# Performance work log

Hardware: AMD Instinct MI355X
Metric: run time of the kernel (lower is better)

The kernel has to match this reference:

```python
import jax, jax.numpy as jnp
import numpy as np

N = 50000    # nodes
E = 600000   # edges
F = 128      # num_features
ED = 16      # edge_dim
H = 4        # heads
D = 32       # per-head channels = hidden_units // heads
HID = H * D  # hidden_units = 128
C = 10       # num_classes


def _lin(k, fan_in, fan_out):
    # torch.nn.Linear-style init scale
    return jax.random.uniform(k, (fan_in, fan_out), jnp.float32, -1.0, 1.0) / np.sqrt(fan_in)


def setup_inputs() -> dict:
    key = jax.random.key(0)
    ks = jax.random.split(key, 24)
    inp = {
        "x": jax.random.normal(ks[0], (N, F), jnp.float32),
        "edge_index": jax.random.randint(ks[1], (2, E), 0, N, dtype=jnp.int32),
        "edge_attr": jax.random.normal(ks[2], (E, ED), jnp.float32),
    }
    j = 3
    for l, ind in enumerate([F, HID]):
        specs = {"q": (ind, HID, True), "k": (ind, HID, True), "v": (ind, HID, True),
                 "e": (ED, HID, False), "s": (ind, HID, True)}
        for nm, (i, o, bias) in specs.items():
            inp[f"W{nm}{l}"] = _lin(ks[j], i, o); j += 1
            if bias:
                inp[f"b{nm}{l}"] = jnp.zeros((o,), jnp.float32)
    inp["Wout"] = _lin(ks[j], HID, C)
    inp["bout"] = jnp.zeros((C,), jnp.float32)
    return inp


def _transformer_conv(x, src, dst, eattr, Wq, bq, Wk, bk, Wv, bv, We, Ws, bs):
    # PyG TransformerConv: concat=True, root_weight=True, beta=False, eval dropout.
    n = x.shape[0]
    q = (x @ Wq + bq).reshape(n, H, D)
    k = (x @ Wk + bk).reshape(n, H, D)
    v = (x @ Wv + bv).reshape(n, H, D)
    e = (eattr @ We).reshape(-1, H, D)           # edge embedding, added to key and value
    kj = k[src] + e                              # [E, H, D]
    vj = v[src] + e                              # [E, H, D]
    logits = jnp.einsum("ehd,ehd->eh", q[dst], kj) / np.sqrt(D)
    m = jax.ops.segment_max(logits, dst, num_segments=n)          # [N, H]
    ex = jnp.exp(logits - m[dst])
    denom = jax.ops.segment_sum(ex, dst, num_segments=n)          # [N, H]
    alpha = ex / (denom[dst] + 1e-16)                             # PyG softmax eps
    out = jax.ops.segment_sum(vj * alpha[..., None], dst, num_segments=n)
    return out.reshape(n, HID) + x @ Ws + bs                      # concat heads + skip


def reference(x, edge_index, edge_attr,
              Wq0, bq0, Wk0, bk0, Wv0, bv0, We0, Ws0, bs0,
              Wq1, bq1, Wk1, bk1, Wv1, bv1, We1, Ws1, bs1,
              Wout, bout):
    src, dst = edge_index[0], edge_index[1]
    h = jax.nn.relu(_transformer_conv(x, src, dst, edge_attr,
                                      Wq0, bq0, Wk0, bk0, Wv0, bv0, We0, Ws0, bs0))
    h = jax.nn.relu(_transformer_conv(h, src, dst, edge_attr,
                                      Wq1, bq1, Wk1, bk1, Wv1, bv1, We1, Ws1, bs1))
    logits = h @ Wout + bout
    return jax.nn.log_softmax(logits, axis=1)
```

## Files before the change

### kernel.cpp

```cpp
#include <hip/hip_runtime.h>

typedef unsigned short u16;
typedef unsigned int u32;
typedef __attribute__((ext_vector_type(4))) u16 u16x4;
typedef __attribute__((ext_vector_type(8))) u16 u16x8;
typedef __attribute__((ext_vector_type(4))) u32 u32x4;
typedef __attribute__((ext_vector_type(8))) short short8;
typedef __attribute__((ext_vector_type(4))) float f32x4;
typedef __attribute__((ext_vector_type(4))) float f4;
typedef __attribute__((ext_vector_type(2))) float f2;

#define NN 50000
#define NE 600000
#define HEADS 4
#define DH 32
#define HIDU 128
#define NC 10
#define NBLK 196
#define WES_T 34
#define WES_H 546

#define SCALE2 0.25503486164f

__device__ __forceinline__ float bf2f(u16 u) {
    union { unsigned int i; float f; } c; c.i = ((unsigned int)u) << 16; return c.f;
}
__device__ __forceinline__ u16 f2bf(float f) {
    union { float f; unsigned int i; } c; c.f = f;
    unsigned int x = c.i;
    return (u16)((x + 0x7fffu + ((x >> 16) & 1u)) >> 16);
}
__device__ __forceinline__ float lo_bf(u32 d) { return __uint_as_float(d << 16); }
__device__ __forceinline__ float hi_bf(u32 d) { return __uint_as_float(d & 0xffff0000u); }
__device__ __forceinline__ float qadd_xor1(float v) {
    int o = __builtin_amdgcn_update_dpp(0, __float_as_int(v), 0xB1, 0xF, 0xF, true);
    return v + __int_as_float(o);
}
__device__ __forceinline__ float qadd_xor2(float v) {
    int o = __builtin_amdgcn_update_dpp(0, __float_as_int(v), 0x4E, 0xF, 0xF, true);
    return v + __int_as_float(o);
}

__global__ void k_zero(int* p, int n) {
    int i = blockIdx.x * blockDim.x + threadIdx.x;
    if (i < n) p[i] = 0;
}

__global__ void k_hist(const int* __restrict__ dst, int* __restrict__ deg) {
    int i = blockIdx.x * blockDim.x + threadIdx.x;
    if (i < NE) atomicAdd(&deg[dst[i]], 1);
}

__global__ __launch_bounds__(256) void scan_a(const int* __restrict__ deg,
                                              int* __restrict__ bsum) {
    __shared__ int red[4];
    int i = blockIdx.x * 256 + threadIdx.x;
    int v = (i < NN) ? deg[i] : 0;
    #pragma unroll
    for (int off = 1; off < 64; off <<= 1) v += __shfl_xor(v, off);
    if ((threadIdx.x & 63) == 0) red[threadIdx.x >> 6] = v;
    __syncthreads();
    if (threadIdx.x == 0) bsum[blockIdx.x] = red[0] + red[1] + red[2] + red[3];
}

__global__ __launch_bounds__(256) void scan_b(const int* __restrict__ bsum,
                                              int* __restrict__ boff,
                                              int* __restrict__ row_ptr,
                                              int* __restrict__ csr_src,
                                              u16* __restrict__ ea16) {
    __shared__ int s[256];
    int t = threadIdx.x;
    int v = (t < NBLK) ? bsum[t] : 0;
    s[t] = v;
    __syncthreads();
    for (int off = 1; off < 256; off <<= 1) {
        int x = (t >= off) ? s[t - off] : 0;
        __syncthreads();
        s[t] += x;
        __syncthreads();
    }
    if (t < NBLK) boff[t] = s[t] - v;
    if (t == 0) row_ptr[NN] = NE;
    if (t < 8)  csr_src[NE + t] = 0;
    if (t < 128) ea16[(size_t)NE * 16 + t] = 0;
}

__global__ __launch_bounds__(256) void scan_c(const int* __restrict__ deg,
                                              const int* __restrict__ boff,
                                              int* __restrict__ row_ptr,
                                              int* __restrict__ cursor) {
    __shared__ int s[256];
    int t = threadIdx.x;
    int i = blockIdx.x * 256 + t;
    int v = (i < NN) ? deg[i] : 0;
    s[t] = v;
    __syncthreads();
    for (int off = 1; off < 256; off <<= 1) {
        int x = (t >= off) ? s[t - off] : 0;
        __syncthreads();
        s[t] += x;
        __syncthreads();
    }
    if (i < NN) {
        int r = boff[blockIdx.x] + s[t] - v;
        row_ptr[i] = r;
        cursor[i] = r;
    }
}

__global__ void k_scatter(const int* __restrict__ ei, const float* __restrict__ eattr,
                          int* __restrict__ cursor,
                          int* __restrict__ csr_src, u16* __restrict__ ea16) {
    int i = blockIdx.x * blockDim.x + threadIdx.x;
    if (i < NE) {
        int s = ei[i];
        int d = ei[NE + i];
        int pos = atomicAdd(&cursor[d], 1);
        csr_src[pos] = s;
        const f4* ep = (const f4*)(eattr + (size_t)i * 16);
        f4 a = ep[0], b = ep[1], c = ep[2], dd = ep[3];
        u16x8 o0, o1;
        #pragma unroll
        for (int j = 0; j < 4; j++) {
            o0[j] = f2bf(a[j]); o0[4 + j] = f2bf(b[j]);
            o1[j] = f2bf(c[j]); o1[4 + j] = f2bf(dd[j]);
        }
        *(u16x8*)(ea16 + (size_t)pos * 16)     = o0;
        *(u16x8*)(ea16 + (size_t)pos * 16 + 8) = o1;
    }
}

__global__ void k_cvtw(const float* w0, const float* w1, const float* w2, const float* w3,
                       const float* w4, const float* w5, const float* w6, const float* w7,
                       u16* __restrict__ hi) {
    const float* w;
    switch (blockIdx.x) {
        case 0: w = w0; break; case 1: w = w1; break;
        case 2: w = w2; break; case 3: w = w3; break;
        case 4: w = w4; break; case 5: w = w5; break;
        case 6: w = w6; break; default: w = w7; break;
    }
    u16* oh = hi + blockIdx.x * 16384;
    #pragma unroll
    for (int i = 0; i < 8; i++) {
        int idx = threadIdx.x + (blockIdx.y * 8 + i) * 256;
        int k = idx >> 7, n = idx & 127;
        oh[n * 128 + k] = f2bf(w[idx]);
    }
}

__global__ __launch_bounds__(256) void gemm_qkvs(
    const float* __restrict__ X, const u16* __restrict__ WtHi,
    const float* __restrict__ b0, const float* __restrict__ b1,
    const float* __restrict__ b2, const float* __restrict__ b3,
    float* __restrict__ outq, u16* __restrict__ outk, u16* __restrict__ outv,
    float* __restrict__ outs, int nrows)
{
    __shared__ u16 Bs[128 * 128];
    const int mat = blockIdx.y;
    const u16* wh = WtHi + mat * 16384;

    #pragma unroll
    for (int i = 0; i < 8; i++) {
        int idx = threadIdx.x + i * 256;
        int n = idx >> 4, g = idx & 15;
        *(u16x8*)(&Bs[n * 128 + ((g ^ (n & 15)) << 3)]) = *(const u16x8*)(wh + n * 128 + g * 8);
    }
    __syncthreads();

    const int wave = threadIdx.x >> 6, lane = threadIdx.x & 63;
    const int n0 = lane & 15;
    const int qw = lane >> 4;
    const int kq = qw * 8;

    const float* xp[2];
    #pragma unroll
    for (int rt = 0; rt < 2; rt++) {
        int arow = blockIdx.x * 128 + wave * 32 + rt * 16 + n0;
        int arow_c = arow < nrows ? arow : nrows - 1;
        xp[rt] = X + (size_t)arow_c * HIDU + kq;
    }

    f32x4 acc[2][8];
    #pragma unroll
    for (int rt = 0; rt < 2; rt++)
        #pragma unroll
        for (int nt = 0; nt < 8; nt++) acc[rt][nt] = (f32x4){0.f, 0.f, 0.f, 0.f};

    #pragma unroll
    for (int ks = 0; ks < 4; ks++) {
        short8 ah[2];
        #pragma unroll
        for (int rt = 0; rt < 2; rt++) {
            f4 a0 = *(const f4*)(xp[rt] + ks * 32);
            f4 a1 = *(const f4*)(xp[rt] + ks * 32 + 4);
            #pragma unroll
            for (int j = 0; j < 4; j++) {
                ah[rt][j]     = (short)(__float_as_uint(a0[j]) >> 16);
                ah[rt][4 + j] = (short)(__float_as_uint(a1[j]) >> 16);
            }
        }
        #pragma unroll
        for (int nt = 0; nt < 8; nt++) {
            const int boff = (nt * 16 + n0) * 128 + (((ks << 2) + qw) ^ n0) * 8;
            short8 bh = *(const short8*)(&Bs[boff]);
            #pragma unroll
            for (int rt = 0; rt < 2; rt++)
                acc[rt][nt] = __builtin_amdgcn_mfma_f32_16x16x32_bf16(ah[rt], bh, acc[rt][nt], 0, 0, 0);
        }
    }

    const float* bia = (mat == 0) ? b0 : (mat == 1) ? b1 : (mat == 2) ? b2 : b3;
    #pragma unroll
    for (int rt = 0; rt < 2; rt++) {
        const int rbase = blockIdx.x * 128 + wave * 32 + rt * 16 + qw * 4;
        #pragma unroll
        for (int nt = 0; nt < 8; nt++) {
            int col = nt * 16 + n0;
            float bv = bia[col];
            #pragma unroll
            for (int r = 0; r < 4; r++) {
                int grow = rbase + r;
                if (grow < nrows) {
                    float v = acc[rt][nt][r] + bv;
                    if (mat == 0)      outq[(size_t)grow * HIDU + col] = v;
                    else if (mat == 1) outk[(size_t)grow * HIDU + col] = f2bf(v);
                    else if (mat == 2) outv[(size_t)grow * HIDU + col] = f2bf(v);
                    else               outs[(size_t)grow * HIDU + col] = v;
                }
            }
        }
    }
}

template<int MODE>
__global__ __launch_bounds__(256) void attn_t(
    const float* __restrict__ qb, const u16* __restrict__ kb, const u16* __restrict__ vb,
    const float* __restrict__ sb, const u16* __restrict__ ea16, const float* __restrict__ We,
    const int* __restrict__ row_ptr, const int* __restrict__ csr_src,
    float* __restrict__ hout_f32,
    const float* __restrict__ Wout, const float* __restrict__ bout,
    float* __restrict__ out_logits)
{
    __shared__ float WeS[4 * WES_H];
    __shared__ float WoT[MODE ? (NC * HIDU) : 1];
    __shared__ float boS[MODE ? NC : 1];

    #pragma unroll
    for (int i = 0; i < 8; i++) {
        int idx = threadIdx.x + i * 256;
        int tt = idx >> 7, c = idx & 127;
        int h = c >> 5, j = c & 31;
        WeS[h * WES_H + tt * WES_T + j] = We[idx];
    }
    if (MODE == 1) {
        #pragma unroll
        for (int i = 0; i < 5; i++) {
            int idx = threadIdx.x + i * 256;
            if (idx < HIDU * NC) {
                int c = idx >> 7, ch = idx & 127;
                WoT[idx] = Wout[ch * NC + c];
            }
        }
        if (threadIdx.x < NC) boS[threadIdx.x] = bout[threadIdx.x];
    }
    __syncthreads();

    int gtid = blockIdx.x * 256 + threadIdx.x;
    int n   = gtid >> 4;
    int l16 = gtid & 15;
    int h   = l16 >> 2;
    int sub = l16 & 3;
    const int lane = threadIdx.x & 63;
    const float* WeH = &WeS[h * WES_H];
    const int j0  = sub * 8;
    const int ch0 = h * DH + j0;
    const int t0  = sub * 4;

    f4 qa, qbv;
    {
        const f4* qp = (const f4*)(qb + (size_t)n * HIDU + ch0);
        qa = qp[0]; qbv = qp[1];
    }

    f4 g4v;
    {
        float part[16];
        #pragma unroll
        for (int t = 0; t < 16; t++) {
            const f2* wp = (const f2*)(WeH + t * WES_T + j0);
            f2 w0 = wp[0], w1 = wp[1], w2 = wp[2], w3 = wp[3];
            part[t] = qa[0] * w0.x + qa[1] * w0.y + qa[2] * w1.x + qa[3] * w1.y
                    + qbv[0] * w2.x + qbv[1] * w2.y + qbv[2] * w3.x + qbv[3] * w3.y;
        }
        #pragma unroll
        for (int t = 0; t < 16; t++) { part[t] = qadd_xor1(part[t]); part[t] = qadd_xor2(part[t]); }
        g4v[0] = part[t0]; g4v[1] = part[t0 + 1]; g4v[2] = part[t0 + 2]; g4v[3] = part[t0 + 3];
    }

    float l = 0.f;
    f4 O0 = {0.f, 0.f, 0.f, 0.f}, O1 = {0.f, 0.f, 0.f, 0.f};
    f4 a4 = {0.f, 0.f, 0.f, 0.f};

    const int r0 = row_ptr[n], r1 = row_ptr[n + 1];

    int s0 = 0, s1 = 0, s2 = 0, s3 = 0;
    u16x4 x0 = {0,0,0,0}, x1 = {0,0,0,0}, x2 = {0,0,0,0}, x3 = {0,0,0,0};
    if (r0 < r1) {
        s0 = csr_src[r0];     s1 = csr_src[r0 + 1];
        s2 = csr_src[r0 + 2]; s3 = csr_src[r0 + 3];
        x0 = *(const u16x4*)(ea16 + (size_t)r0 * 16 + t0);
        x1 = *(const u16x4*)(ea16 + (size_t)(r0 + 1) * 16 + t0);
        x2 = *(const u16x4*)(ea16 + (size_t)(r0 + 2) * 16 + t0);
        x3 = *(const u16x4*)(ea16 + (size_t)(r0 + 3) * 16 + t0);
    }

    for (int e = r0; e < r1; e += 4) {
        u32x4 k0 = *(const u32x4*)(kb + (size_t)s0 * HIDU + ch0);
        u32x4 k1 = *(const u32x4*)(kb + (size_t)s1 * HIDU + ch0);
        u32x4 k2 = *(const u32x4*)(kb + (size_t)s2 * HIDU + ch0);
        u32x4 k3 = *(const u32x4*)(kb + (size_t)s3 * HIDU + ch0);
        u32x4 v0 = *(const u32x4*)(vb + (size_t)s0 * HIDU + ch0);
        u32x4 v1 = *(const u32x4*)(vb + (size_t)s1 * HIDU + ch0);
        u32x4 v2 = *(const u32x4*)(vb + (size_t)s2 * HIDU + ch0);
        u32x4 v3 = *(const u32x4*)(vb + (size_t)s3 * HIDU + ch0);
        int ns0 = csr_src[e + 4], ns1 = csr_src[e + 5];
        int ns2 = csr_src[e + 6], ns3 = csr_src[e + 7];
        u16x4 nx0 = *(const u16x4*)(ea16 + (size_t)(e + 4) * 16 + t0);
        u16x4 nx1 = *(const u16x4*)(ea16 + (size_t)(e + 5) * 16 + t0);
        u16x4 nx2 = *(const u16x4*)(ea16 + (size_t)(e + 6) * 16 + t0);
        u16x4 nx3 = *(const u16x4*)(ea16 + (size_t)(e + 7) * 16 + t0);

        f4 ea0 = {bf2f(x0[0]), bf2f(x0[1]), bf2f(x0[2]), bf2f(x0[3])};
        f4 ea1 = {bf2f(x1[0]), bf2f(x1[1]), bf2f(x1[2]), bf2f(x1[3])};
        f4 ea2 = {bf2f(x2[0]), bf2f(x2[1]), bf2f(x2[2]), bf2f(x2[3])};
        f4 ea3 = {bf2f(x3[0]), bf2f(x3[1]), bf2f(x3[2]), bf2f(x3[3])};

        f4 ac0 = qa * (f4){lo_bf(k0[0]), hi_bf(k0[0]), lo_bf(k0[1]), hi_bf(k0[1])}
               + qbv * (f4){lo_bf(k0[2]), hi_bf(k0[2]), lo_bf(k0[3]), hi_bf(k0[3])}
               + g4v * ea0;
        f4 ac1 = qa * (f4){lo_bf(k1[0]), hi_bf(k1[0]), lo_bf(k1[1]), hi_bf(k1[1])}
               + qbv * (f4){lo_bf(k1[2]), hi_bf(k1[2]), lo_bf(k1[3]), hi_bf(k1[3])}
               + g4v * ea1;
        f4 ac2 = qa * (f4){lo_bf(k2[0]), hi_bf(k2[0]), lo_bf(k2[1]), hi_bf(k2[1])}
               + qbv * (f4){lo_bf(k2[2]), hi_bf(k2[2]), lo_bf(k2[3]), hi_bf(k2[3])}
               + g4v * ea2;
        f4 ac3 = qa * (f4){lo_bf(k3[0]), hi_bf(k3[0]), lo_bf(k3[1]), hi_bf(k3[1])}
               + qbv * (f4){lo_bf(k3[2]), hi_bf(k3[2]), lo_bf(k3[3]), hi_bf(k3[3])}
               + g4v * ea3;
        float d0 = (ac0[0] + ac0[1]) + (ac0[2] + ac0[3]);
        float d1 = (ac1[0] + ac1[1]) + (ac1[2] + ac1[3]);
        float d2 = (ac2[0] + ac2[1]) + (ac2[2] + ac2[3]);
        float d3 = (ac3[0] + ac3[1]) + (ac3[2] + ac3[3]);
        d0 = qadd_xor1(d0); d1 = qadd_xor1(d1); d2 = qadd_xor1(d2); d3 = qadd_xor1(d3);
        d0 = qadd_xor2(d0); d1 = qadd_xor2(d1); d2 = qadd_xor2(d2); d3 = qadd_xor2(d3);

        float w0 = exp2f(d0 * SCALE2);
        float w1 = (e + 1 < r1) ? exp2f(d1 * SCALE2) : 0.f;
        float w2 = (e + 2 < r1) ? exp2f(d2 * SCALE2) : 0.f;
        float w3 = (e + 3 < r1) ? exp2f(d3 * SCALE2) : 0.f;
        l += (w0 + w1) + (w2 + w3);

        O0 = O0
           + (f4){lo_bf(v0[0]), hi_bf(v0[0]), lo_bf(v0[1]), hi_bf(v0[1])} * w0
           + (f4){lo_bf(v1[0]), hi_bf(v1[0]), lo_bf(v1[1]), hi_bf(v1[1])} * w1
           + (f4){lo_bf(v2[0]), hi_bf(v2[0]), lo_bf(v2[1]), hi_bf(v2[1])} * w2
           + (f4){lo_bf(v3[0]), hi_bf(v3[0]), lo_bf(v3[1]), hi_bf(v3[1])} * w3;
        O1 = O1
           + (f4){lo_bf(v0[2]), hi_bf(v0[2]), lo_bf(v0[3]), hi_bf(v0[3])} * w0
           + (f4){lo_bf(v1[2]), hi_bf(v1[2]), lo_bf(v1[3]), hi_bf(v1[3])} * w1
           + (f4){lo_bf(v2[2]), hi_bf(v2[2]), lo_bf(v2[3]), hi_bf(v2[3])} * w2
           + (f4){lo_bf(v3[2]), hi_bf(v3[2]), lo_bf(v3[3]), hi_bf(v3[3])} * w3;
        a4 = a4 + ea0 * w0 + ea1 * w1 + ea2 * w2 + ea3 * w3;

        s0 = ns0; s1 = ns1; s2 = ns2; s3 = ns3;
        x0 = nx0; x1 = nx1; x2 = nx2; x3 = nx3;
    }

    float af[16];
    #pragma unroll
    for (int t = 0; t < 16; t++)
        af[t] = __shfl(a4[t & 3], (lane & ~3) | (t >> 2));

    float invl = 1.0f / (l + 1e-16f);
    const f4* sp = (const f4*)(sb + (size_t)n * HIDU + ch0);
    f4 sp0 = sp[0], sp1 = sp[1];

    f4 evA = {0.f, 0.f, 0.f, 0.f}, evB = {0.f, 0.f, 0.f, 0.f};
    #pragma unroll
    for (int t = 0; t < 16; t++) {
        float a = af[t];
        const f2* wp = (const f2*)(WeH + t * WES_T + j0);
        f2 w0 = wp[0], w1 = wp[1], w2 = wp[2], w3 = wp[3];
        evA[0] += a * w0.x; evA[1] += a * w0.y; evA[2] += a * w1.x; evA[3] += a * w1.y;
        evB[0] += a * w2.x; evB[1] += a * w2.y; evB[2] += a * w3.x; evB[3] += a * w3.y;
    }

    f4 val0, val1;
    #pragma unroll
    for (int j = 0; j < 4; j++) {
        val0[j] = fmaxf((O0[j] + evA[j]) * invl + sp0[j], 0.f);
        val1[j] = fmaxf((O1[j] + evB[j]) * invl + sp1[j], 0.f);
    }

    if (MODE == 0) {
        const size_t obase = (size_t)n * HIDU + ch0;
        *(f4*)(hout_f32 + obase) = val0;
        *(f4*)(hout_f32 + obase + 4) = val1;
    } else {
        float plg[NC];
        #pragma unroll
        for (int c = 0; c < NC; c++) {
            const f4* wr = (const f4*)(WoT + c * HIDU + ch0);
            f4 wa = wr[0], wb = wr[1];
            plg[c] = val0[0] * wa[0] + val0[1] * wa[1] + val0[2] * wa[2] + val0[3] * wa[3]
                   + val1[0] * wb[0] + val1[1] * wb[1] + val1[2] * wb[2] + val1[3] * wb[3];
        }
        #pragma unroll
        for (int mask = 1; mask < 16; mask <<= 1) {
            #pragma unroll
            for (int c = 0; c < NC; c++) plg[c] += __shfl_xor(plg[c], mask);
        }
        float lg[NC];
        float mx = -INFINITY;
        #pragma unroll
        for (int c = 0; c < NC; c++) { lg[c] = plg[c] + boS[c]; mx = fmaxf(mx, lg[c]); }
        float sum = 0.f;
        #pragma unroll
        for (int c = 0; c < NC; c++) sum += __expf(lg[c] - mx);
        float lse = mx + __logf(sum);
        if (l16 < NC) out_logits[(size_t)n * NC + l16] = lg[l16] - lse;
    }
}

extern "C" void kernel_launch(void* const* d_in, const int* in_sizes, int n_in,
                              void* d_out, int out_size, void* d_ws, size_t ws_size,
                              hipStream_t stream) {
    const float* x     = (const float*)d_in[0];
    const int*   ei    = (const int*)d_in[1];
    const float* eattr = (const float*)d_in[2];
    const float *Wq0 = (const float*)d_in[3],  *bq0 = (const float*)d_in[4];
    const float *Wk0 = (const float*)d_in[5],  *bk0 = (const float*)d_in[6];
    const float *Wv0 = (const float*)d_in[7],  *bv0 = (const float*)d_in[8];
    const float *We0 = (const float*)d_in[9];
    const float *Ws0 = (const float*)d_in[10], *bs0 = (const float*)d_in[11];
    const float *Wq1 = (const float*)d_in[12], *bq1 = (const float*)d_in[13];
    const float *Wk1 = (const float*)d_in[14], *bk1 = (const float*)d_in[15];
    const float *Wv1 = (const float*)d_in[16], *bv1 = (const float*)d_in[17];
    const float *We1 = (const float*)d_in[18];
    const float *Ws1 = (const float*)d_in[19], *bs1 = (const float*)d_in[20];
    const float *Wout = (const float*)d_in[21], *bout = (const float*)d_in[22];

    char* p = (char*)d_ws;
    auto alloc = [&](size_t bytes) -> void* {
        void* r = (void*)p;
        p += (bytes + 255) & ~(size_t)255;
        return r;
    };
    int* deg      = (int*)alloc(NN * 4);
    int* row_ptr  = (int*)alloc((NN + 1) * 4);
    int* cursor   = (int*)alloc(NN * 4);
    int* bsum     = (int*)alloc(NBLK * 4);
    int* boff     = (int*)alloc(NBLK * 4);
    int* csr_src  = (int*)alloc(((size_t)NE + 8) * 4);
    float* qb     = (float*)alloc((size_t)NN * HIDU * 4);
    u16* kb       = (u16*)alloc((size_t)NN * HIDU * 2);
    u16* vb       = (u16*)alloc((size_t)NN * HIDU * 2);
    float* sbuf   = (float*)alloc((size_t)NN * HIDU * 4);
    float* hbuf   = (float*)alloc((size_t)NN * HIDU * 4);
    u16* ea16     = (u16*)alloc(((size_t)NE + 8) * 16 * 2);
    u16* wthi     = (u16*)alloc(8 * 16384 * 2);

    k_zero<<<(NN + 255) / 256, 256, 0, stream>>>(deg, NN);
    k_hist<<<(NE + 255) / 256, 256, 0, stream>>>(ei + NE, deg);
    scan_a<<<NBLK, 256, 0, stream>>>(deg, bsum);
    scan_b<<<1, 256, 0, stream>>>(bsum, boff, row_ptr, csr_src, ea16);
    scan_c<<<NBLK, 256, 0, stream>>>(deg, boff, row_ptr, cursor);
    k_scatter<<<(NE + 255) / 256, 256, 0, stream>>>(ei, eattr, cursor, csr_src, ea16);

    k_cvtw<<<dim3(8, 8), 256, 0, stream>>>(Wq0, Wk0, Wv0, Ws0, Wq1, Wk1, Wv1, Ws1, wthi);

    const int gm = (NN + 127) / 128;
    const int ga = (NN * 16) / 256;

    gemm_qkvs<<<dim3(gm, 4), 256, 0, stream>>>(x, wthi, bq0, bk0, bv0, bs0,
                                               qb, kb, vb, sbuf, NN);
    attn_t<0><<<ga, 256, 0, stream>>>(qb, kb, vb, sbuf, ea16, We0, row_ptr, csr_src,
                                      hbuf, nullptr, nullptr, nullptr);
    gemm_qkvs<<<dim3(gm, 4), 256, 0, stream>>>(hbuf, wthi + 4 * 16384, bq1, bk1, bv1, bs1,
                                               qb, kb, vb, sbuf, NN);
    attn_t<1><<<ga, 256, 0, stream>>>(qb, kb, vb, sbuf, ea16, We1, row_ptr, csr_src,
                                      nullptr, Wout, bout, (float*)d_out);
}
```

Measured before the change: 434.7 us.

## Interleave K and V rows, drop software prefetch, raise attention occupancy

K and V projections are now written into one interleaved bf16 buffer (256 halves per node), so each gathered source node's K and V slices share a row and DRAM pages. The attention loop drops its one-iteration-ahead software prefetch of csr_src and edge attributes and instead clamps out-of-range tail indices to the current edge, which removes the padding writes in scan_b. The attention kernel also gets a launch bound of 8 blocks per CU to push occupancy, which limits registers and risks spills. Without the prefetch, hiding latency depends more on that higher occupancy.

```diff
diff --git a/kernel.cpp b/kernel.cpp
--- a/kernel.cpp
+++ b/kernel.cpp
@@ -19,6 +19,7 @@
 #define NBLK 196
 #define WES_T 34
 #define WES_H 546
+#define KVS 256
 
 #define SCALE2 0.25503486164f
 
@@ -65,9 +66,7 @@
 
 __global__ __launch_bounds__(256) void scan_b(const int* __restrict__ bsum,
                                               int* __restrict__ boff,
-                                              int* __restrict__ row_ptr,
-                                              int* __restrict__ csr_src,
-                                              u16* __restrict__ ea16) {
+                                              int* __restrict__ row_ptr) {
     __shared__ int s[256];
     int t = threadIdx.x;
     int v = (t < NBLK) ? bsum[t] : 0;
@@ -81,8 +80,6 @@
     }
     if (t < NBLK) boff[t] = s[t] - v;
     if (t == 0) row_ptr[NN] = NE;
-    if (t < 8)  csr_src[NE + t] = 0;
-    if (t < 128) ea16[(size_t)NE * 16 + t] = 0;
 }
 
 __global__ __launch_bounds__(256) void scan_c(const int* __restrict__ deg,
@@ -153,7 +150,7 @@
     const float* __restrict__ X, const u16* __restrict__ WtHi,
     const float* __restrict__ b0, const float* __restrict__ b1,
     const float* __restrict__ b2, const float* __restrict__ b3,
-    float* __restrict__ outq, u16* __restrict__ outk, u16* __restrict__ outv,
+    float* __restrict__ outq, u16* __restrict__ kvb,
     float* __restrict__ outs, int nrows)
 {
     __shared__ u16 Bs[128 * 128];
@@ -224,8 +221,8 @@
                 if (grow < nrows) {
                     float v = acc[rt][nt][r] + bv;
                     if (mat == 0)      outq[(size_t)grow * HIDU + col] = v;
-                    else if (mat == 1) outk[(size_t)grow * HIDU + col] = f2bf(v);
-                    else if (mat == 2) outv[(size_t)grow * HIDU + col] = f2bf(v);
+                    else if (mat == 1) kvb[(size_t)grow * KVS + col] = f2bf(v);
+                    else if (mat == 2) kvb[(size_t)grow * KVS + 128 + col] = f2bf(v);
                     else               outs[(size_t)grow * HIDU + col] = v;
                 }
             }
@@ -234,8 +231,8 @@
 }
 
 template<int MODE>
-__global__ __launch_bounds__(256) void attn_t(
-    const float* __restrict__ qb, const u16* __restrict__ kb, const u16* __restrict__ vb,
+__global__ __launch_bounds__(256, 8) void attn_t(
+    const float* __restrict__ qb, const u16* __restrict__ kvb,
     const float* __restrict__ sb, const u16* __restrict__ ea16, const float* __restrict__ We,
     const int* __restrict__ row_ptr, const int* __restrict__ csr_src,
     float* __restrict__ hout_f32,
@@ -304,32 +301,27 @@
 
     const int r0 = row_ptr[n], r1 = row_ptr[n + 1];
 
-    int s0 = 0, s1 = 0, s2 = 0, s3 = 0;
-    u16x4 x0 = {0,0,0,0}, x1 = {0,0,0,0}, x2 = {0,0,0,0}, x3 = {0,0,0,0};
-    if (r0 < r1) {
-        s0 = csr_src[r0];     s1 = csr_src[r0 + 1];
-        s2 = csr_src[r0 + 2]; s3 = csr_src[r0 + 3];
-        x0 = *(const u16x4*)(ea16 + (size_t)r0 * 16 + t0);
-        x1 = *(const u16x4*)(ea16 + (size_t)(r0 + 1) * 16 + t0);
-        x2 = *(const u16x4*)(ea16 + (size_t)(r0 + 2) * 16 + t0);
-        x3 = *(const u16x4*)(ea16 + (size_t)(r0 + 3) * 16 + t0);
-    }
-
     for (int e = r0; e < r1; e += 4) {
-        u32x4 k0 = *(const u32x4*)(kb + (size_t)s0 * HIDU + ch0);
-        u32x4 k1 = *(const u32x4*)(kb + (size_t)s1 * HIDU + ch0);
-        u32x4 k2 = *(const u32x4*)(kb + (size_t)s2 * HIDU + ch0);
-        u32x4 k3 = *(const u32x4*)(kb + (size_t)s3 * HIDU + ch0);
-        u32x4 v0 = *(const u32x4*)(vb + (size_t)s0 * HIDU + ch0);
-        u32x4 v1 = *(const u32x4*)(vb + (size_t)s1 * HIDU + ch0);
-        u32x4 v2 = *(const u32x4*)(vb + (size_t)s2 * HIDU + ch0);
-        u32x4 v3 = *(const u32x4*)(vb + (size_t)s3 * HIDU + ch0);
-        int ns0 = csr_src[e + 4], ns1 = csr_src[e + 5];
-        int ns2 = csr_src[e + 6], ns3 = csr_src[e + 7];
-        u16x4 nx0 = *(const u16x4*)(ea16 + (size_t)(e + 4) * 16 + t0);
-        u16x4 nx1 = *(const u16x4*)(ea16 + (size_t)(e + 5) * 16 + t0);
-        u16x4 nx2 = *(const u16x4*)(ea16 + (size_t)(e + 6) * 16 + t0);
-        u16x4 nx3 = *(const u16x4*)(ea16 + (size_t)(e + 7) * 16 + t0);
+        const int e1 = (e + 1 < r1) ? e + 1 : e;
+        const int e2 = (e + 2 < r1) ? e + 2 : e;
+        const int e3 = (e + 3 < r1) ? e + 3 : e;
+        int s0 = csr_src[e], s1 = csr_src[e1], s2 = csr_src[e2], s3 = csr_src[e3];
+        u16x4 x0 = *(const u16x4*)(ea16 + (size_t)e  * 16 + t0);
+        u16x4 x1 = *(const u16x4*)(ea16 + (size_t)e1 * 16 + t0);
+        u16x4 x2 = *(const u16x4*)(ea16 + (size_t)e2 * 16 + t0);
+        u16x4 x3 = *(const u16x4*)(ea16 + (size_t)e3 * 16 + t0);
+        const u16* p0 = kvb + (size_t)s0 * KVS + ch0;
+        const u16* p1 = kvb + (size_t)s1 * KVS + ch0;
+        const u16* p2 = kvb + (size_t)s2 * KVS + ch0;
+        const u16* p3 = kvb + (size_t)s3 * KVS + ch0;
+        u32x4 k0 = *(const u32x4*)(p0);
+        u32x4 k1 = *(const u32x4*)(p1);
+        u32x4 k2 = *(const u32x4*)(p2);
+        u32x4 k3 = *(const u32x4*)(p3);
+        u32x4 v0 = *(const u32x4*)(p0 + 128);
+        u32x4 v1 = *(const u32x4*)(p1 + 128);
+        u32x4 v2 = *(const u32x4*)(p2 + 128);
+        u32x4 v3 = *(const u32x4*)(p3 + 128);
 
         f4 ea0 = {bf2f(x0[0]), bf2f(x0[1]), bf2f(x0[2]), bf2f(x0[3])};
         f4 ea1 = {bf2f(x1[0]), bf2f(x1[1]), bf2f(x1[2]), bf2f(x1[3])};
@@ -372,9 +364,6 @@
            + (f4){lo_bf(v2[2]), hi_bf(v2[2]), lo_bf(v2[3]), hi_bf(v2[3])} * w2
            + (f4){lo_bf(v3[2]), hi_bf(v3[2]), lo_bf(v3[3]), hi_bf(v3[3])} * w3;
         a4 = a4 + ea0 * w0 + ea1 * w1 + ea2 * w2 + ea3 * w3;
-
-        s0 = ns0; s1 = ns1; s2 = ns2; s3 = ns3;
-        x0 = nx0; x1 = nx1; x2 = nx2; x3 = nx3;
     }
 
     float af[16];
@@ -462,19 +451,18 @@
     int* cursor   = (int*)alloc(NN * 4);
     int* bsum     = (int*)alloc(NBLK * 4);
     int* boff     = (int*)alloc(NBLK * 4);
-    int* csr_src  = (int*)alloc(((size_t)NE + 8) * 4);
+    int* csr_src  = (int*)alloc((size_t)NE * 4);
     float* qb     = (float*)alloc((size_t)NN * HIDU * 4);
-    u16* kb       = (u16*)alloc((size_t)NN * HIDU * 2);
-    u16* vb       = (u16*)alloc((size_t)NN * HIDU * 2);
+    u16* kvb      = (u16*)alloc((size_t)NN * KVS * 2);
     float* sbuf   = (float*)alloc((size_t)NN * HIDU * 4);
     float* hbuf   = (float*)alloc((size_t)NN * HIDU * 4);
-    u16* ea16     = (u16*)alloc(((size_t)NE + 8) * 16 * 2);
+    u16* ea16     = (u16*)alloc((size_t)NE * 16 * 2);
     u16* wthi     = (u16*)alloc(8 * 16384 * 2);
 
     k_zero<<<(NN + 255) / 256, 256, 0, stream>>>(deg, NN);
     k_hist<<<(NE + 255) / 256, 256, 0, stream>>>(ei + NE, deg);
     scan_a<<<NBLK, 256, 0, stream>>>(deg, bsum);
-    scan_b<<<1, 256, 0, stream>>>(bsum, boff, row_ptr, csr_src, ea16);
+    scan_b<<<1, 256, 0, stream>>>(bsum, boff, row_ptr);
     scan_c<<<NBLK, 256, 0, stream>>>(deg, boff, row_ptr, cursor);
     k_scatter<<<(NE + 255) / 256, 256, 0, stream>>>(ei, eattr, cursor, csr_src, ea16);
 
@@ -484,11 +472,11 @@
     const int ga = (NN * 16) / 256;
 
     gemm_qkvs<<<dim3(gm, 4), 256, 0, stream>>>(x, wthi, bq0, bk0, bv0, bs0,
-                                               qb, kb, vb, sbuf, NN);
-    attn_t<0><<<ga, 256, 0, stream>>>(qb, kb, vb, sbuf, ea16, We0, row_ptr, csr_src,
+                                               qb, kvb, sbuf, NN);
+    attn_t<0><<<ga, 256, 0, stream>>>(qb, kvb, sbuf, ea16, We0, row_ptr, csr_src,
                                       hbuf, nullptr, nullptr, nullptr);
     gemm_qkvs<<<dim3(gm, 4), 256, 0, stream>>>(hbuf, wthi + 4 * 16384, bq1, bk1, bv1, bs1,
-                                               qb, kb, vb, sbuf, NN);
-    attn_t<1><<<ga, 256, 0, stream>>>(qb, kb, vb, sbuf, ea16, We1, row_ptr, csr_src,
+                                               qb, kvb, sbuf, NN);
+    attn_t<1><<<ga, 256, 0, stream>>>(qb, kvb, sbuf, ea16, We1, row_ptr, csr_src,
                                       nullptr, Wout, bout, (float*)d_out);
 }
```

Result: slower. 644.1 us (+48.2%).
